# Kernel tuning notes

Measured on AMD Instinct MI355X. Metric: run time of the kernel, lower is better.

Reference implementation:

```python
import jax, jax.numpy as jnp
import numpy as np

B, T, I, H, L, O = 64, 512, 256, 1024, 2, 512


def setup_inputs() -> dict:
    key = jax.random.key(0)
    ks = jax.random.split(key, 11)
    sc = 1.0 / np.sqrt(H).astype(np.float32)
    r = lambda k, shape: jax.random.normal(k, shape, jnp.float32) * sc
    return {
        "x": jax.random.normal(ks[0], (B, T, I), jnp.float32),
        "Wih0": r(ks[1], (H, I)),
        "Whh0": r(ks[2], (H, H)),
        "bih0": r(ks[3], (H,)),
        "bhh0": r(ks[4], (H,)),
        "Wih1": r(ks[5], (H, H)),
        "Whh1": r(ks[6], (H, H)),
        "bih1": r(ks[7], (H,)),
        "bhh1": r(ks[8], (H,)),
        "Wfc": r(ks[9], (O, H)),
        "bfc": r(ks[10], (O,)),
    }


def _rnn_layer(x, Wih, Whh, bih, bhh):
    # x: [B, T, D] -> hidden sequence [B, T, H]; tanh RNN (PyTorch nn.RNN semantics)
    # Precompute the input projection for all timesteps (one big GEMM),
    # leaving only the recurrent GEMM inside the scan.
    xp = jnp.einsum('btd,hd->bth', x, Wih) + bih + bhh  # [B, T, H]
    h0 = jnp.zeros((x.shape[0], Whh.shape[0]), x.dtype)

    def step(h, xt):  # xt: [B, H]
        h = jnp.tanh(xt + h @ Whh.T)
        return h, h

    _, hs = jax.lax.scan(step, h0, jnp.swapaxes(xp, 0, 1))  # [T, B, H]
    return jnp.swapaxes(hs, 0, 1)  # [B, T, H]


def reference(x, Wih0, Whh0, bih0, bhh0, Wih1, Whh1, bih1, bhh1, Wfc, bfc):
    h1 = _rnn_layer(x, Wih0, Whh0, bih0, bhh0)
    h2 = _rnn_layer(h1, Wih1, Whh1, bih1, bhh1)
    last = h2[:, -1, :]                     # [B, H]
    return last @ Wfc.T + bfc               # [B, O]
```

## Files before the change

kernel.cpp:

```cpp
#include <hip/hip_runtime.h>
#include <cmath>

#define BB 64
#define TT 512
#define II 256
#define HH 1024
#define OO 512
#define LAG 24

typedef short bf8 __attribute__((ext_vector_type(8)));
typedef float f32x4 __attribute__((ext_vector_type(4)));
typedef unsigned long long u64;

#define MFMA(a, b, c) __builtin_amdgcn_mfma_f32_16x16x32_bf16((a), (b), (c), 0, 0, 0)

__device__ __forceinline__ unsigned short f2bf(float f) {
    unsigned u = __float_as_uint(f);
    return (unsigned short)((u + 0x7fffu + ((u >> 16) & 1u)) >> 16);
}
__device__ __forceinline__ float bf2f(unsigned short h) {
    return __uint_as_float((unsigned)h << 16);
}
__device__ __forceinline__ void split8(const float* v, bf8& hi, bf8& lo) {
#pragma unroll
    for (int j = 0; j < 8; ++j) {
        unsigned short h = f2bf(v[j]);
        float r = v[j] - bf2f(h);
        hi[j] = (short)h;
        lo[j] = (short)f2bf(r);
    }
}
__device__ __forceinline__ void ld8(float* v, const float* p) {
    *(float4*)v       = *(const float4*)p;
    *(float4*)(v + 4) = *(const float4*)(p + 4);
}
__device__ __forceinline__ bf8 load_h(const void* p) { return *(const bf8*)p; }
__device__ __forceinline__ void store_h16(void* p, u64 a, u64 b) {
    __hip_atomic_store((u64*)p, a, __ATOMIC_RELAXED, __HIP_MEMORY_SCOPE_AGENT);
    __hip_atomic_store((u64*)((char*)p + 8), b, __ATOMIC_RELAXED, __HIP_MEMORY_SCOPE_AGENT);
}
__device__ __forceinline__ unsigned ld_flag(const void* p) {
    return __hip_atomic_load((const unsigned*)p, __ATOMIC_RELAXED, __HIP_MEMORY_SCOPE_AGENT);
}
__device__ __forceinline__ void st_flag(void* p, unsigned v) {
    __hip_atomic_store((unsigned*)p, v, __ATOMIC_RELAXED, __HIP_MEMORY_SCOPE_AGENT);
}
__device__ __forceinline__ void acquire_fence() {
    __builtin_amdgcn_fence(__ATOMIC_ACQUIRE, "agent");
    asm volatile("" ::: "memory");
}

__global__ __launch_bounds__(512, 1) void rnn_lag3(
    const float* __restrict__ x,
    const float* __restrict__ Wih0, const float* __restrict__ Whh0,
    const float* __restrict__ bih0, const float* __restrict__ bhh0,
    const float* __restrict__ Wih1, const float* __restrict__ Whh1,
    const float* __restrict__ bih1, const float* __restrict__ bhh1,
    const float* __restrict__ Wfc,  const float* __restrict__ bfc,
    float* __restrict__ out, float* __restrict__ ws,
    int sm, int fpm)
{
    __shared__ float shmem[5120];
    char* staging = (char*)(shmem + 4608);

    const int tid  = threadIdx.x;
    const int w    = tid >> 6;
    const int lane = tid & 63;
    const int col  = lane & 15;
    const int kg   = lane >> 4;
    const int bid  = blockIdx.x;
    const int grp   = bid & 3;
    const int layer = (bid >> 2) & 1;
    const int slot  = bid >> 3;
    const int rb    = slot * 32;
    const int b0    = grp * 16;

    char* wsB    = (char*)ws;
    char* fA     = wsB;
    char* fB     = wsB + 2048;
    char* h1base = wsB + 4096;
    char* h2base = h1base + (size_t)(sm + 1) * 4 * 65536;

    bf8 wh[2][8], wl[2][8];
    {
        float v[8];
        if (layer == 0) {
            #pragma unroll
            for (int n = 0; n < 2; ++n) {
                ld8(v, Wih0 + (size_t)(rb + n * 16 + col) * II + (w * 32 + kg * 8));
                split8(v, wh[n][4], wl[n][4]);
                #pragma unroll
                for (int c = 0; c < 4; ++c) {
                    ld8(v, Whh0 + (size_t)(rb + n * 16 + col) * HH + ((w * 4 + c) * 32 + kg * 8));
                    split8(v, wh[n][c], wl[n][c]);
                }
            }
        } else {
            #pragma unroll
            for (int n = 0; n < 2; ++n)
                #pragma unroll
                for (int c = 0; c < 4; ++c) {
                    ld8(v, Wih1 + (size_t)(rb + n * 16 + col) * HH + ((w * 4 + c) * 32 + kg * 8));
                    split8(v, wh[n][c], wl[n][c]);
                    ld8(v, Whh1 + (size_t)(rb + n * 16 + col) * HH + ((w * 4 + c) * 32 + kg * 8));
                    split8(v, wh[n][4 + c], wl[n][4 + c]);
                }
        }
    }

    const int n_  = tid >> 8;
    const int ekk = (tid >> 4) & 15;
    const int eb  = tid & 15;
    const int R   = rb + n_ * 16 + ekk;
    const float bsum = layer ? (bih1[R] + bhh1[R]) : (bih0[R] + bhh0[R]);
    const int kk5 = n_ * 16 + ekk;
    const int stg = (eb + 16 * (kk5 >> 3)) * 32 + (kk5 & 7) * 2;

    acquire_fence();

    float xv[8];
    if (layer == 0)
        ld8(xv, x + (size_t)(b0 + col) * TT * II + (w * 32 + kg * 8));

    for (int t = 0; t < TT; ++t) {
        if ((t & fpm) == 0) acquire_fence();

        f32x4 acc0 = {0.f, 0.f, 0.f, 0.f};
        f32x4 acc1 = {0.f, 0.f, 0.f, 0.f};

        if (layer == 0) {
            bf8 xh, xl;
            split8(xv, xh, xl);
            acc0 = MFMA(xh, wh[0][4], acc0); acc0 = MFMA(xh, wl[0][4], acc0);
            acc0 = MFMA(xl, wh[0][4], acc0);
            acc1 = MFMA(xh, wh[1][4], acc1); acc1 = MFMA(xh, wl[1][4], acc1);
            acc1 = MFMA(xl, wh[1][4], acc1);

            if (w == 0) {
                const char* fp = (lane < 32 ? fA : fB)
                               + (size_t)(grp * 32 + (lane & 31)) * 16;
                const int tgt = (lane < 32) ? t : (t - LAG);
                for (;;) {
                    int f = (int)ld_flag(fp);
                    if (__all(f >= tgt)) break;
                }
            }
            __syncthreads();

            if (t >= 1) {
                const char* h1r = h1base + (size_t)(((t - 1) & sm) * 4 + grp) * 65536;
                #pragma unroll
                for (int c = 0; c < 4; ++c) {
                    const char* p = h1r + (size_t)(w * 4 + c) * 2048 + lane * 32;
                    bf8 hh = load_h(p), hl = load_h(p + 16);
                    acc0 = MFMA(hh, wh[0][c], acc0); acc0 = MFMA(hh, wl[0][c], acc0);
                    acc0 = MFMA(hl, wh[0][c], acc0);
                    acc1 = MFMA(hh, wh[1][c], acc1); acc1 = MFMA(hh, wl[1][c], acc1);
                    acc1 = MFMA(hl, wh[1][c], acc1);
                }
            }
        } else {
            if (w == 0) {
                const char* fp = fA + (size_t)(grp * 32 + (lane & 31)) * 16;
                const int tgt = t + 1;
                for (;;) {
                    int f = (lane < 32) ? (int)ld_flag(fp) : tgt;
                    if (__all(f >= tgt)) break;
                }
            }
            __syncthreads();
            {
                const char* h1r = h1base + (size_t)((t & sm) * 4 + grp) * 65536;
                #pragma unroll
                for (int c = 0; c < 4; ++c) {
                    const char* p = h1r + (size_t)(w * 4 + c) * 2048 + lane * 32;
                    bf8 hh = load_h(p), hl = load_h(p + 16);
                    acc0 = MFMA(hh, wh[0][c], acc0); acc0 = MFMA(hh, wl[0][c], acc0);
                    acc0 = MFMA(hl, wh[0][c], acc0);
                    acc1 = MFMA(hh, wh[1][c], acc1); acc1 = MFMA(hh, wl[1][c], acc1);
                    acc1 = MFMA(hl, wh[1][c], acc1);
                }
            }
            if (t >= 1) {
                if (w == 0) {
                    const char* fp = fB + (size_t)(grp * 32 + (lane & 31)) * 16;
                    const int tgt = t;
                    for (;;) {
                        int f = (lane < 32) ? (int)ld_flag(fp) : tgt;
                        if (__all(f >= tgt)) break;
                    }
                }
                __syncthreads();
                const char* h2r = h2base + (size_t)(((t - 1) & sm) * 4 + grp) * 65536;
                #pragma unroll
                for (int c = 0; c < 4; ++c) {
                    const char* p = h2r + (size_t)(w * 4 + c) * 2048 + lane * 32;
                    bf8 hh = load_h(p), hl = load_h(p + 16);
                    acc0 = MFMA(hh, wh[0][4 + c], acc0); acc0 = MFMA(hh, wl[0][4 + c], acc0);
                    acc0 = MFMA(hl, wh[0][4 + c], acc0);
                    acc1 = MFMA(hh, wh[1][4 + c], acc1); acc1 = MFMA(hh, wl[1][4 + c], acc1);
                    acc1 = MFMA(hl, wh[1][4 + c], acc1);
                }
            }
        }

        #pragma unroll
        for (int r = 0; r < 4; ++r) {
            shmem[(w * 2 + 0) * 288 + (kg * 4 + r) * 18 + col] = acc0[r];
            shmem[(w * 2 + 1) * 288 + (kg * 4 + r) * 18 + col] = acc1[r];
        }
        __syncthreads();

        {
            float s = bsum;
            #pragma unroll
            for (int wv = 0; wv < 8; ++wv)
                s += shmem[(wv * 2 + n_) * 288 + eb * 18 + ekk];
            const float val = tanhf(s);
            const unsigned short hi = f2bf(val);
            const unsigned short lo = f2bf(val - bf2f(hi));
            *(unsigned short*)(staging + stg)      = hi;
            *(unsigned short*)(staging + stg + 16) = lo;
        }
        __syncthreads();

        {
            char* hw = (layer ? h2base : h1base)
                     + (size_t)((t & sm) * 4 + grp) * 65536 + (size_t)slot * 2048;
            if (tid < 128) {
                const char* src = staging + tid * 16;
                store_h16(hw + tid * 16, *(const u64*)src, *(const u64*)(src + 8));
            }
        }
        asm volatile("s_waitcnt vmcnt(0)" ::: "memory");
        __syncthreads();
        if (tid == 0)
            st_flag((layer ? fB : fA) + (size_t)(grp * 32 + slot) * 16, (unsigned)(t + 1));

        if (layer == 0 && t + 1 < TT)
            ld8(xv, x + ((size_t)(b0 + col) * TT + (t + 1)) * II + (w * 32 + kg * 8));
    }

    if (tid < 128) {
        while ((int)ld_flag(fB + (size_t)tid * 16) < TT)
            __builtin_amdgcn_s_sleep(2);
    }
    __syncthreads();
    acquire_fence();

    float* Wlds = shmem + 2560;
    ((float4*)Wlds)[tid] = ((const float4*)(Wfc + (size_t)(2 * bid) * HH))[tid];
    __syncthreads();

    float p0 = 0.f, p1 = 0.f;
    {
        const int gr   = lane >> 4;
        const int bsub = lane & 15;
        const char* hb = h2base + (size_t)(((TT - 1) & sm) * 4 + gr) * 65536;
        #pragma unroll 4
        for (int k8 = w * 16; k8 < w * 16 + 16; ++k8) {
            const char* p = hb + (size_t)(k8 >> 2) * 2048
                          + (size_t)(bsub + ((k8 & 3) << 4)) * 32;
            bf8 hi = load_h(p), lo = load_h(p + 16);
            const int kb = k8 * 8;
            #pragma unroll
            for (int j = 0; j < 8; ++j) {
                float f = bf2f((unsigned short)hi[j]) + bf2f((unsigned short)lo[j]);
                p0 += f * Wlds[kb + j];
                p1 += f * Wlds[1024 + kb + j];
            }
        }
    }
    __syncthreads();
    shmem[(w * 64 + lane) * 2 + 0] = p0;
    shmem[(w * 64 + lane) * 2 + 1] = p1;
    __syncthreads();
    if (w < 2) {
        float s = bfc[2 * bid + w];
        #pragma unroll
        for (int j = 0; j < 8; ++j) s += shmem[(j * 64 + lane) * 2 + w];
        out[(size_t)lane * OO + 2 * bid + w] = s;
    }
}

extern "C" void kernel_launch(void* const* d_in, const int* in_sizes, int n_in,
                              void* d_out, int out_size, void* d_ws, size_t ws_size,
                              hipStream_t stream) {
    const float* x    = (const float*)d_in[0];
    const float* Wih0 = (const float*)d_in[1];
    const float* Whh0 = (const float*)d_in[2];
    const float* bih0 = (const float*)d_in[3];
    const float* bhh0 = (const float*)d_in[4];
    const float* Wih1 = (const float*)d_in[5];
    const float* Whh1 = (const float*)d_in[6];
    const float* bih1 = (const float*)d_in[7];
    const float* bhh1 = (const float*)d_in[8];
    const float* Wfc  = (const float*)d_in[9];
    const float* bfc  = (const float*)d_in[10];
    float* out = (float*)d_out;
    float* ws  = (float*)d_ws;

    int depth = 32;
    if (ws_size >= (size_t)4096 + (size_t)2 * 128 * 4 * 65536)      depth = 128;
    else if (ws_size >= (size_t)4096 + (size_t)2 * 64 * 4 * 65536)  depth = 64;
    int sm  = depth - 1;
    int fpm = depth / 2 - 1;

    hipMemsetAsync(d_ws, 0, 4096, stream);

    void* args[] = { (void*)&x,
                     (void*)&Wih0, (void*)&Whh0, (void*)&bih0, (void*)&bhh0,
                     (void*)&Wih1, (void*)&Whh1, (void*)&bih1, (void*)&bhh1,
                     (void*)&Wfc,  (void*)&bfc,  (void*)&out,  (void*)&ws,
                     (void*)&sm,   (void*)&fpm };
    hipLaunchCooperativeKernel((void*)rnn_lag3, dim3(256), dim3(512),
                               args, 0, stream);
}
```

Before: 2.291 ms.

## Replace block-wide flag barrier with per-wave targeted flag polling

Each wave now polls only the four producer flags for the h-chunks it actually reads, replacing the wave-0 poll plus __syncthreads, so waves can proceed independently. The layer-0 back-pressure check on layer 1 progress runs only every 8 steps with a lag derived from ring depth, and the ring buffer depth can grow to 256 when the workspace allows. This aims to cut per-timestep barrier latency on the serial critical path. It risks subtle ordering bugs, since only a compiler barrier remains, and more polling traffic from all waves.

```diff
diff --git a/kernel.cpp b/kernel.cpp
--- a/kernel.cpp
+++ b/kernel.cpp
@@ -6,7 +6,6 @@
 #define II 256
 #define HH 1024
 #define OO 512
-#define LAG 24
 
 typedef short bf8 __attribute__((ext_vector_type(8)));
 typedef float f32x4 __attribute__((ext_vector_type(4)));
@@ -50,7 +49,7 @@
     asm volatile("" ::: "memory");
 }
 
-__global__ __launch_bounds__(512, 1) void rnn_lag3(
+__global__ __launch_bounds__(512, 1) void rnn_lag4(
     const float* __restrict__ x,
     const float* __restrict__ Wih0, const float* __restrict__ Whh0,
     const float* __restrict__ bih0, const float* __restrict__ bhh0,
@@ -58,7 +57,7 @@
     const float* __restrict__ bih1, const float* __restrict__ bhh1,
     const float* __restrict__ Wfc,  const float* __restrict__ bfc,
     float* __restrict__ out, float* __restrict__ ws,
-    int sm, int fpm)
+    int sm, int fpm, int lag)
 {
     __shared__ float shmem[5120];
     char* staging = (char*)(shmem + 4608);
@@ -136,16 +135,23 @@
             acc1 = MFMA(xh, wh[1][4], acc1); acc1 = MFMA(xh, wl[1][4], acc1);
             acc1 = MFMA(xl, wh[1][4], acc1);
 
-            if (w == 0) {
+            {
+                const char* fp = fA + (size_t)(grp * 32 + (w * 4 + (lane & 3))) * 16;
+                for (;;) {
+                    int f = (lane < 4) ? (int)ld_flag(fp) : 0x7fffffff;
+                    if (__all(f >= t)) break;
+                }
+            }
+            if ((t & 7) == 0 && w == 0) {
                 const char* fp = (lane < 32 ? fA : fB)
                                + (size_t)(grp * 32 + (lane & 31)) * 16;
-                const int tgt = (lane < 32) ? t : (t - LAG);
+                const int tgt = t + 7 - lag;
                 for (;;) {
                     int f = (int)ld_flag(fp);
                     if (__all(f >= tgt)) break;
                 }
             }
-            __syncthreads();
+            asm volatile("" ::: "memory");
 
             if (t >= 1) {
                 const char* h1r = h1base + (size_t)(((t - 1) & sm) * 4 + grp) * 65536;
@@ -160,15 +166,18 @@
                 }
             }
         } else {
-            if (w == 0) {
-                const char* fp = fA + (size_t)(grp * 32 + (lane & 31)) * 16;
-                const int tgt = t + 1;
+            {
+                const int pc = lane & 3;
+                const char* fp = (lane < 4 ? fA : fB)
+                               + (size_t)(grp * 32 + (w * 4 + pc)) * 16;
+                const int tgt = (lane < 4) ? (t + 1) : t;
                 for (;;) {
-                    int f = (lane < 32) ? (int)ld_flag(fp) : tgt;
+                    int f = (lane < 8) ? (int)ld_flag(fp) : 0x7fffffff;
                     if (__all(f >= tgt)) break;
                 }
             }
-            __syncthreads();
+            asm volatile("" ::: "memory");
+
             {
                 const char* h1r = h1base + (size_t)((t & sm) * 4 + grp) * 65536;
                 #pragma unroll
@@ -182,15 +191,6 @@
                 }
             }
             if (t >= 1) {
-                if (w == 0) {
-                    const char* fp = fB + (size_t)(grp * 32 + (lane & 31)) * 16;
-                    const int tgt = t;
-                    for (;;) {
-                        int f = (lane < 32) ? (int)ld_flag(fp) : tgt;
-                        if (__all(f >= tgt)) break;
-                    }
-                }
-                __syncthreads();
                 const char* h2r = h2base + (size_t)(((t - 1) & sm) * 4 + grp) * 65536;
                 #pragma unroll
                 for (int c = 0; c < 4; ++c) {
@@ -301,10 +301,12 @@
     float* ws  = (float*)d_ws;
 
     int depth = 32;
-    if (ws_size >= (size_t)4096 + (size_t)2 * 128 * 4 * 65536)      depth = 128;
+    if (ws_size >= (size_t)4096 + (size_t)2 * 256 * 4 * 65536)      depth = 256;
+    else if (ws_size >= (size_t)4096 + (size_t)2 * 128 * 4 * 65536) depth = 128;
     else if (ws_size >= (size_t)4096 + (size_t)2 * 64 * 4 * 65536)  depth = 64;
     int sm  = depth - 1;
     int fpm = depth / 2 - 1;
+    int lag = depth - 12;
 
     hipMemsetAsync(d_ws, 0, 4096, stream);
 
@@ -312,7 +314,7 @@
                      (void*)&Wih0, (void*)&Whh0, (void*)&bih0, (void*)&bhh0,
                      (void*)&Wih1, (void*)&Whh1, (void*)&bih1, (void*)&bhh1,
                      (void*)&Wfc,  (void*)&bfc,  (void*)&out,  (void*)&ws,
-                     (void*)&sm,   (void*)&fpm };
-    hipLaunchCooperativeKernel((void*)rnn_lag3, dim3(256), dim3(512),
+                     (void*)&sm,   (void*)&fpm,  (void*)&lag };
+    hipLaunchCooperativeKernel((void*)rnn_lag4, dim3(256), dim3(512),
                                args, 0, stream);
 }
```

Result: slower. 2.763 ms (+20.6%).
